# Performance work log

Measured on AMD Instinct MI355X. Metric: run time of the kernel, lower is better.

Reference implementation:

```python
import jax, jax.numpy as jnp
import numpy as np


def setup_inputs() -> dict:
    key = jax.random.key(0)
    k1, k2 = jax.random.split(key)
    B, C, N, M = 8, 3, 4096, 4096
    source_point_cloud = jax.random.normal(k1, (B, C, N), dtype=jnp.float32)
    target_point_cloud = jax.random.normal(k2, (B, C, M), dtype=jnp.float32)
    return {"source_point_cloud": source_point_cloud,
            "target_point_cloud": target_point_cloud}


def _nn_indices(source, target):
    # source: [B,3,N], target: [B,3,M]
    # squared Euclidean distance: |s|^2 + |t|^2 - 2 s.t  (monotone in true distance,
    # so argmin matches the KD-tree nearest-neighbor query)
    s2 = jnp.sum(source * source, axis=1)               # [B,N]
    t2 = jnp.sum(target * target, axis=1)               # [B,M]
    cross = jnp.einsum('bcn,bcm->bnm', source, target)  # [B,N,M]
    d2 = s2[:, :, None] + t2[:, None, :] - 2.0 * cross  # [B,N,M]
    return jnp.argmin(d2, axis=2)                       # [B,N]


def reference(source_point_cloud, target_point_cloud):
    # Per-batch: nearest target point for each source point, then mean MSE.
    idx = _nn_indices(source_point_cloud, target_point_cloud)        # [B,N]
    # gather matched target points: [B,3,N]
    matched = jnp.take_along_axis(target_point_cloud, idx[:, None, :], axis=2)
    diff = source_point_cloud - matched
    # MSELoss over the (1,3,N) batch slice -> mean over 3*N elements; one scalar per batch
    loss_per_batch = jnp.mean(diff * diff, axis=(1, 2))              # [B]
    return loss_per_batch
```

## Files before the change

### kernel.cpp

```cpp
#include <hip/hip_runtime.h>


#define B_ 8
#define N_ 4096
#define CH 4096
#define BS 12288
#define TQ 256
#define NE 16
#define BIG 3.4e38f

__global__ __launch_bounds__(512, 8)
void nn_loss_main(const float* __restrict__ src,
                  const float* __restrict__ tgt,
                  float* __restrict__ partial) {
    __shared__ __align__(16) char smem[8 * 512 * 4];
    float4* stage = (float4*)smem;
    float*  red   = (float*)smem;

    const int tid  = threadIdx.x;
    const int blk  = blockIdx.x;
    const int b    = blk >> 7;
    const int e    = (blk >> 3) & 15;
    const int sgrp = blk & 7;
    const int ls   = tid & 63;
    const int w    = tid >> 6;

    if (tid < TQ) {
        const float* tb = tgt + b * BS;
        const int m = (e << 8) + tid;
        float x = tb[m], y = tb[m + CH], z = tb[m + 2 * CH];
        stage[tid] = make_float4(x, y, z, x * x + y * y + z * z);
    }

    const float* sb = src + b * BS;
    float ax[8], ay[8], az[8];
    #pragma unroll
    for (int j = 0; j < 8; ++j) {
        int n = (sgrp << 9) + (j << 6) + ls;
        ax[j] = -2.0f * sb[n];
        ay[j] = -2.0f * sb[n + CH];
        az[j] = -2.0f * sb[n + 2 * CH];
    }

    __syncthreads();

    float best[8];
    #pragma unroll
    for (int j = 0; j < 8; ++j) best[j] = BIG;

    const float4* tp = stage + (w << 5);
    #pragma unroll 2
    for (int i = 0; i < 32; i += 2) {
        float4 t0 = tp[i];
        float4 t1 = tp[i + 1];
        #pragma unroll
        for (int j = 0; j < 8; ++j) {
            float d0 = fmaf(ax[j], t0.x, fmaf(ay[j], t0.y, fmaf(az[j], t0.z, t0.w)));
            float d1 = fmaf(ax[j], t1.x, fmaf(ay[j], t1.y, fmaf(az[j], t1.z, t1.w)));
            best[j] = fminf(fminf(best[j], d0), d1);
        }
    }

    __syncthreads();

    #pragma unroll
    for (int j = 0; j < 8; ++j) {
        float s2 = 0.25f * fmaf(ax[j], ax[j], fmaf(ay[j], ay[j], az[j] * az[j]));
        red[(w << 9) + (j << 6) + ls] = best[j] + s2;
    }

    __syncthreads();

    float mn = red[tid];
    #pragma unroll
    for (int v = 1; v < 8; ++v)
        mn = fminf(mn, red[(v << 9) + tid]);
    partial[(e << 15) + (b << 12) + (sgrp << 9) + tid] = mn;
}

__global__ __launch_bounds__(512)
void reduce_kernel(const float* __restrict__ partial,
                   float* __restrict__ out) {
    const int blk = blockIdx.x;
    const int b   = blk >> 3;
    const int g   = blk & 7;
    const int tid = threadIdx.x;
    const int ls  = tid & 63;
    const int w   = tid >> 6;

    const int base = (b << 12) + (g << 9) + tid;
    float mn = partial[base];
    #pragma unroll
    for (int e = 1; e < NE; ++e)
        mn = fminf(mn, partial[(e << 15) + base]);

    #pragma unroll
    for (int off = 32; off > 0; off >>= 1)
        mn += __shfl_down(mn, off, 64);

    __shared__ float red[8];
    if (ls == 0) red[w] = mn;
    __syncthreads();
    if (tid == 0) {
        float s = 0.0f;
        #pragma unroll
        for (int k = 0; k < 8; ++k) s += red[k];
        atomicAdd(&out[b], s * (1.0f / (3.0f * (float)N_)));
    }
}

extern "C" void kernel_launch(void* const* d_in, const int* in_sizes, int n_in,
                              void* d_out, int out_size, void* d_ws, size_t ws_size,
                              hipStream_t stream) {
    const float* src = (const float*)d_in[0];
    const float* tgt = (const float*)d_in[1];
    float* out = (float*)d_out;
    float* partial = (float*)d_ws;

    hipMemsetAsync(out, 0, B_ * sizeof(float), stream);
    nn_loss_main<<<1024, 512, 0, stream>>>(src, tgt, partial);
    reduce_kernel<<<64, 512, 0, stream>>>(partial, out);
}
```

Baseline: 70.00 us.

## Fold output zeroing into main kernel, vectorize source loads, resize reduce grid

```diff
diff --git a/kernel.cpp b/kernel.cpp
--- a/kernel.cpp
+++ b/kernel.cpp
@@ -12,7 +12,8 @@
 __global__ __launch_bounds__(512, 8)
 void nn_loss_main(const float* __restrict__ src,
                   const float* __restrict__ tgt,
-                  float* __restrict__ partial) {
+                  float* __restrict__ partial,
+                  float* __restrict__ out) {
     __shared__ __align__(16) char smem[8 * 512 * 4];
     float4* stage = (float4*)smem;
     float*  red   = (float*)smem;
@@ -25,6 +26,16 @@
     const int ls   = tid & 63;
     const int w    = tid >> 6;
 
+    if (blk == 0 && tid < B_) out[tid] = 0.0f;
+
+    const float* sb = src + b * BS + (sgrp << 9);
+    const float4* sx4 = (const float4*)sb;
+    const float4* sy4 = (const float4*)(sb + CH);
+    const float4* sz4 = (const float4*)(sb + 2 * CH);
+    float4 x0 = sx4[ls * 2], x1 = sx4[ls * 2 + 1];
+    float4 y0 = sy4[ls * 2], y1 = sy4[ls * 2 + 1];
+    float4 z0 = sz4[ls * 2], z1 = sz4[ls * 2 + 1];
+
     if (tid < TQ) {
         const float* tb = tgt + b * BS;
         const int m = (e << 8) + tid;
@@ -32,15 +43,13 @@
         stage[tid] = make_float4(x, y, z, x * x + y * y + z * z);
     }
 
-    const float* sb = src + b * BS;
     float ax[8], ay[8], az[8];
-    #pragma unroll
-    for (int j = 0; j < 8; ++j) {
-        int n = (sgrp << 9) + (j << 6) + ls;
-        ax[j] = -2.0f * sb[n];
-        ay[j] = -2.0f * sb[n + CH];
-        az[j] = -2.0f * sb[n + 2 * CH];
-    }
+    ax[0] = -2.0f * x0.x; ax[1] = -2.0f * x0.y; ax[2] = -2.0f * x0.z; ax[3] = -2.0f * x0.w;
+    ax[4] = -2.0f * x1.x; ax[5] = -2.0f * x1.y; ax[6] = -2.0f * x1.z; ax[7] = -2.0f * x1.w;
+    ay[0] = -2.0f * y0.x; ay[1] = -2.0f * y0.y; ay[2] = -2.0f * y0.z; ay[3] = -2.0f * y0.w;
+    ay[4] = -2.0f * y1.x; ay[5] = -2.0f * y1.y; ay[6] = -2.0f * y1.z; ay[7] = -2.0f * y1.w;
+    az[0] = -2.0f * z0.x; az[1] = -2.0f * z0.y; az[2] = -2.0f * z0.z; az[3] = -2.0f * z0.w;
+    az[4] = -2.0f * z1.x; az[5] = -2.0f * z1.y; az[6] = -2.0f * z1.z; az[7] = -2.0f * z1.w;
 
     __syncthreads();
 
@@ -66,7 +75,7 @@
     #pragma unroll
     for (int j = 0; j < 8; ++j) {
         float s2 = 0.25f * fmaf(ax[j], ax[j], fmaf(ay[j], ay[j], az[j] * az[j]));
-        red[(w << 9) + (j << 6) + ls] = best[j] + s2;
+        red[(w << 9) + (ls << 3) + j] = best[j] + s2;
     }
 
     __syncthreads();
@@ -78,17 +87,17 @@
     partial[(e << 15) + (b << 12) + (sgrp << 9) + tid] = mn;
 }
 
-__global__ __launch_bounds__(512)
+__global__ __launch_bounds__(256)
 void reduce_kernel(const float* __restrict__ partial,
                    float* __restrict__ out) {
     const int blk = blockIdx.x;
-    const int b   = blk >> 3;
-    const int g   = blk & 7;
+    const int b   = blk >> 4;
+    const int c   = blk & 15;
     const int tid = threadIdx.x;
     const int ls  = tid & 63;
     const int w   = tid >> 6;
 
-    const int base = (b << 12) + (g << 9) + tid;
+    const int base = (b << 12) + (c << 8) + tid;
     float mn = partial[base];
     #pragma unroll
     for (int e = 1; e < NE; ++e)
@@ -98,13 +107,11 @@
     for (int off = 32; off > 0; off >>= 1)
         mn += __shfl_down(mn, off, 64);
 
-    __shared__ float red[8];
+    __shared__ float red[4];
     if (ls == 0) red[w] = mn;
     __syncthreads();
     if (tid == 0) {
-        float s = 0.0f;
-        #pragma unroll
-        for (int k = 0; k < 8; ++k) s += red[k];
+        float s = (red[0] + red[1]) + (red[2] + red[3]);
         atomicAdd(&out[b], s * (1.0f / (3.0f * (float)N_)));
     }
 }
@@ -117,7 +124,6 @@
     float* out = (float*)d_out;
     float* partial = (float*)d_ws;
 
-    hipMemsetAsync(out, 0, B_ * sizeof(float), stream);
-    nn_loss_main<<<1024, 512, 0, stream>>>(src, tgt, partial);
-    reduce_kernel<<<64, 512, 0, stream>>>(partial, out);
+    nn_loss_main<<<1024, 512, 0, stream>>>(src, tgt, partial, out);
+    reduce_kernel<<<128, 256, 0, stream>>>(partial, out);
 }
```

After: 68.25 us. 2.5% less time.
